# Kernel tuning notes

Measured on AMD Instinct MI355X. Metric: run time of the kernel, lower is better.

The kernel has to match this reference:

```python
import jax, jax.numpy as jnp
import numpy as np
from jax import lax

B, H, L, N, COUT = 16, 128, 8192, 16, 128
NEG_SLOPE = 0.3
BN_EPS = 1e-5


def setup_inputs() -> dict:
    key = jax.random.key(0)
    ks = jax.random.split(key, 20)
    x = jax.random.normal(ks[0], (B, H, L), dtype=jnp.float32)
    # --- S4D parameters ---
    log_dt = jnp.log(0.001) + jax.random.uniform(ks[1], (H,), dtype=jnp.float32) * (jnp.log(0.1) - jnp.log(0.001))
    A_log = jnp.log(0.5 * jnp.ones((H, N), dtype=jnp.float32))  # real part magnitude
    A_imag = jnp.broadcast_to(np.pi * jnp.arange(N, dtype=jnp.float32), (H, N)).copy()
    B_re = jnp.ones((H, N), dtype=jnp.float32)
    B_im = jnp.zeros((H, N), dtype=jnp.float32)
    C_re = jax.random.normal(ks[2], (H, N), dtype=jnp.float32) * (0.5 ** 0.5)
    C_im = jax.random.normal(ks[3], (H, N), dtype=jnp.float32) * (0.5 ** 0.5)
    D = jax.random.normal(ks[4], (H,), dtype=jnp.float32)
    # --- dilated conv branches (kernel_size=3, stride=4) ---
    wscale = 1.0 / np.sqrt(H * 3)
    w1 = jax.random.normal(ks[5], (COUT, H, 3), dtype=jnp.float32) * wscale
    b1 = jnp.zeros((COUT,), dtype=jnp.float32)
    w2 = jax.random.normal(ks[6], (COUT, H, 3), dtype=jnp.float32) * wscale
    b2 = jnp.zeros((COUT,), dtype=jnp.float32)
    w3 = jax.random.normal(ks[7], (COUT, H, 3), dtype=jnp.float32) * wscale
    b3 = jnp.zeros((COUT,), dtype=jnp.float32)
    w4 = jax.random.normal(ks[8], (COUT, H, 3), dtype=jnp.float32) * wscale
    b4 = jnp.zeros((COUT,), dtype=jnp.float32)
    gamma = jnp.ones((COUT,), dtype=jnp.float32)
    beta = jnp.zeros((COUT,), dtype=jnp.float32)
    return dict(x=x, log_dt=log_dt, A_log=A_log, A_imag=A_imag, B_re=B_re, B_im=B_im,
                C_re=C_re, C_im=C_im, D=D, w1=w1, b1=b1, w2=w2, b2=b2, w3=w3, b3=b3,
                w4=w4, b4=b4, gamma=gamma, beta=beta)


def _s4d(x, log_dt, A_log, A_imag, B_re, B_im, C_re, C_im, D):
    # x: (B,H,L). S4D with ZOH discretization, FFT long convolution.
    Lx = x.shape[-1]
    dt = jnp.exp(log_dt)[:, None]                    # (H,1)
    A = -jnp.exp(A_log) + 1j * A_imag                # (H,N)
    dtA = dt * A                                     # (H,N)
    dB = (jnp.exp(dtA) - 1.0) / A * (B_re + 1j * B_im)
    CB = (C_re + 1j * C_im) * dB                     # (H,N)
    l = jnp.arange(Lx, dtype=jnp.float32)
    vand = jnp.exp(dtA[:, :, None] * l)              # (H,N,L) Vandermonde
    K = 2.0 * jnp.real(jnp.einsum('hn,hnl->hl', CB, vand))  # (H,L)
    n = 2 * Lx
    Uf = jnp.fft.rfft(x, n=n)                        # (B,H,L+1)
    Kf = jnp.fft.rfft(K, n=n)                        # (H,L+1)
    y = jnp.fft.irfft(Uf * Kf, n=n)[..., :Lx]
    return y + D[:, None] * x


def _dconv(x, w, b, dil, pad):
    y = lax.conv_general_dilated(x, w, window_strides=(4,), padding=[(pad, pad)],
                                 rhs_dilation=(dil,), dimension_numbers=('NCH', 'OIH', 'NCH'))
    return y + b[:, None]


def _bn(z, gamma, beta):
    # training-mode BatchNorm1d: batch stats over (B, L_out) per channel
    m = jnp.mean(z, axis=(0, 2), keepdims=True)
    v = jnp.var(z, axis=(0, 2), keepdims=True)
    return gamma[:, None] * (z - m) * lax.rsqrt(v + BN_EPS) + beta[:, None]


def _lrelu(z):
    return jnp.where(z >= 0, z, NEG_SLOPE * z)


def reference(x, log_dt, A_log, A_imag, B_re, B_im, C_re, C_im, D,
              w1, b1, w2, b2, w3, b3, w4, b4, gamma, beta):
    y = _s4d(x, log_dt, A_log, A_imag, B_re, B_im, C_re, C_im, D)
    d1 = _bn(_dconv(y, w1, b1, 1, 1), gamma, beta)                 # no activation on branch 1
    d2 = _bn(_lrelu(_dconv(y, w2, b2, 2, 2)), gamma, beta)
    d3 = _bn(_lrelu(_dconv(y, w3, b3, 4, 4)), gamma, beta)
    d4 = _bn(_lrelu(_dconv(y, w4, b4, 8, 8)), gamma, beta)
    return jnp.concatenate([d1, d2, d3, d4], axis=1)               # (B, 4*COUT, L//4)
```

## Files before the change

### kernel.cpp

```cpp
#include <hip/hip_runtime.h>
#include <math.h>

typedef unsigned short u16x8 __attribute__((ext_vector_type(8)));
typedef unsigned short u16x2 __attribute__((ext_vector_type(2)));
typedef short s16x8 __attribute__((ext_vector_type(8)));
typedef float f32x4 __attribute__((ext_vector_type(4)));

__device__ __forceinline__ float bf2f(unsigned short u) {
    union { unsigned int i; float f; } v; v.i = ((unsigned int)u) << 16; return v.f;
}
__device__ __forceinline__ unsigned short f2bf(float f) {
    union { unsigned int i; float f; } v; v.f = f;
    unsigned int r = v.i + 0x7FFFu + ((v.i >> 16) & 1u);
    return (unsigned short)(r >> 16);
}

#define MATS_OFF 16384
#define WB_OFF   548864
#define STAT_OFF 942080
#define Y_OFF    1048576
#define YT_OFF   34603008
#define Z_OFF    Y_OFF

__global__ void precompute_s4d(const float* __restrict__ log_dt,
                               const float* __restrict__ A_log,
                               const float* __restrict__ A_imag,
                               const float* __restrict__ B_re,
                               const float* __restrict__ B_im,
                               const float* __restrict__ C_re,
                               const float* __restrict__ C_im,
                               float* __restrict__ w32,
                               unsigned short* __restrict__ MATS)
{
    const int h = blockIdx.x;
    const int tid = threadIdx.x;
    const double dt = exp((double)log_dt[h]);

    #pragma unroll 1
    for (int it = 0; it < 4; it++) {
        int idx = tid + (it << 8);
        int s = idx >> 5, i = idx & 31;
        int n = s >> 1;
        double Ar = -exp((double)A_log[h * 16 + n]);
        double Ai = (double)A_imag[h * 16 + n];
        double dr = dt * Ar, di = dt * Ai;
        double l = (double)(31 - i);
        double e = exp(l * dr);
        double val = (s & 1) ? e * sin(l * di) : e * cos(l * di);
        MATS[(size_t)h * 2080 + s * 32 + i] = f2bf((float)val);
    }
    #pragma unroll 1
    for (int it = 0; it < 4; it++) {
        int idx = tid + (it << 8);
        int j = idx >> 5, s = idx & 31;
        int n = s >> 1;
        double Ar = -exp((double)A_log[h * 16 + n]);
        double Ai = (double)A_imag[h * 16 + n];
        double dr = dt * Ar, di = dt * Ai;
        double ew = exp(dr);
        double wr = ew * cos(di), wi = ew * sin(di);
        double nr = wr - 1.0, ni = wi;
        double inv = 1.0 / (Ar * Ar + Ai * Ai);
        double tr = (nr * Ar + ni * Ai) * inv;
        double ti = (ni * Ar - nr * Ai) * inv;
        double Br = (double)B_re[h * 16 + n], Bi = (double)B_im[h * 16 + n];
        double dbr = tr * Br - ti * Bi, dbi = tr * Bi + ti * Br;
        double Cr = (double)C_re[h * 16 + n], Ci = (double)C_im[h * 16 + n];
        double cbr = Cr * dbr - Ci * dbi, cbi = Cr * dbi + Ci * dbr;
        double m = (double)(j + 1);
        double e = exp(m * dr);
        double pr = e * cos(m * di), pi = e * sin(m * di);
        double gr = cbr * pr - cbi * pi, gi = cbr * pi + cbi * pr;
        double val = (s & 1) ? -2.0 * gi : 2.0 * gr;
        MATS[(size_t)h * 2080 + 1024 + j * 32 + s] = f2bf((float)val);
    }
    if (tid < 32) {
        double l = (double)tid;
        double acc = 0.0;
        for (int n = 0; n < 16; n++) {
            double Ar = -exp((double)A_log[h * 16 + n]);
            double Ai = (double)A_imag[h * 16 + n];
            double dr = dt * Ar, di = dt * Ai;
            double ew = exp(dr);
            double wr = ew * cos(di), wi = ew * sin(di);
            double nr = wr - 1.0, ni = wi;
            double inv = 1.0 / (Ar * Ar + Ai * Ai);
            double tr = (nr * Ar + ni * Ai) * inv;
            double ti = (ni * Ar - nr * Ai) * inv;
            double Br = (double)B_re[h * 16 + n], Bi = (double)B_im[h * 16 + n];
            double dbr = tr * Br - ti * Bi, dbi = tr * Bi + ti * Br;
            double Cr = (double)C_re[h * 16 + n], Ci = (double)C_im[h * 16 + n];
            double cbr = Cr * dbr - Ci * dbi, cbi = Cr * dbi + Ci * dbr;
            double e = exp(l * dr);
            double wlr = e * cos(l * di), wli = e * sin(l * di);
            acc += cbr * wlr - cbi * wli;
        }
        MATS[(size_t)h * 2080 + 2048 + tid] = f2bf((float)(2.0 * acc));
    }
    if (tid < 16) {
        int n = tid;
        double Ar = -exp((double)A_log[h * 16 + n]);
        double Ai = (double)A_imag[h * 16 + n];
        double dr = dt * Ar, di = dt * Ai;
        double e = exp(32.0 * dr);
        w32[h * 32 + 2 * n]     = (float)(e * cos(32.0 * di));
        w32[h * 32 + 2 * n + 1] = (float)(e * sin(32.0 * di));
    }
}

__global__ void wpack(const float* __restrict__ w1, const float* __restrict__ w2,
                      const float* __restrict__ w3, const float* __restrict__ w4,
                      unsigned short* __restrict__ WB)
{
    int idx = blockIdx.x * 256 + threadIdx.x;
    int br = idx / 49152;
    int r  = idx - br * 49152;
    int co = r / 384;
    int k  = r - co * 384;
    int tap = k >> 7, h = k & 127;
    const float* wp = (br == 0) ? w1 : (br == 1) ? w2 : (br == 2) ? w3 : w4;
    WB[idx] = f2bf(wp[co * 384 + h * 3 + tap]);
}

__global__ __launch_bounds__(256, 2) void s4d_mfma(const float* __restrict__ x,
                                                   const float* __restrict__ w32,
                                                   const unsigned short* __restrict__ MATS,
                                                   const float* __restrict__ Dp,
                                                   unsigned short* __restrict__ yout)
{
    __shared__ unsigned short sXc[256 * 40];
    __shared__ unsigned short sM[3840];
    __shared__ float spow2[256];
    __shared__ unsigned short skr[32];
    __shared__ float scratch[8448];
    const int tid = threadIdx.x;
    const int bh = blockIdx.x;
    const int h = bh & 127;
    const int lane = tid & 63, w = tid >> 6;
    const int ml = lane & 15, kg = lane >> 4;

    float xr[32];
    const float4* xp4 = (const float4*)(x + ((size_t)bh << 13) + (tid << 5));
    #pragma unroll
    for (int i = 0; i < 8; i++) {
        float4 v = xp4[i];
        xr[4 * i] = v.x; xr[4 * i + 1] = v.y; xr[4 * i + 2] = v.z; xr[4 * i + 3] = v.w;
    }
    #pragma unroll
    for (int g = 0; g < 4; g++) {
        u16x8 pk;
        #pragma unroll
        for (int e = 0; e < 8; e++) pk[e] = f2bf(xr[g * 8 + e]);
        *(u16x8*)&sXc[tid * 40 + g * 8] = pk;
    }
    {
        int matv = tid >> 7, r = (tid >> 2) & 31, sg = tid & 3;
        u16x8 v = *(const u16x8*)(MATS + (size_t)h * 2080 + matv * 1024 + r * 32 + sg * 8);
        *(u16x8*)&sM[matv * 2560 + r * 40 + sg * 8] = v;
    }
    if (tid < 4) {
        u16x8 v = *(const u16x8*)(MATS + (size_t)h * 2080 + 2048 + tid * 8);
        *(u16x8*)&skr[tid * 8] = v;
    }
    if (tid < 16) {
        float rr = w32[h * 32 + 2 * tid], ii = w32[h * 32 + 2 * tid + 1];
        #pragma unroll
        for (int k = 0; k < 8; k++) {
            spow2[k * 32 + 2 * tid] = rr; spow2[k * 32 + 2 * tid + 1] = ii;
            float n2r = rr * rr - ii * ii, n2i = 2.f * rr * ii;
            rr = n2r; ii = n2i;
        }
    }
    __syncthreads();
    #pragma unroll
    for (int it = 0; it < 4; it++) {
        int idx = tid + (it << 8);
        int j = idx >> 5, i = idx & 31;
        sM[1280 + j * 40 + i] = (i <= j) ? skr[j - i] : (unsigned short)0;
    }
    __syncthreads();

    f32x4 acc[2][4];
    #pragma unroll
    for (int mt = 0; mt < 2; mt++)
        #pragma unroll
        for (int nt = 0; nt < 4; nt++) acc[mt][nt] = (f32x4)(0.f);
    {
        s16x8 af[2], bfr[4];
        #pragma unroll
        for (int mt = 0; mt < 2; mt++)
            af[mt] = *(const s16x8*)&sM[(mt * 16 + ml) * 40 + kg * 8];
        #pragma unroll
        for (int nt = 0; nt < 4; nt++)
            bfr[nt] = *(const s16x8*)&sXc[(w * 64 + nt * 16 + ml) * 40 + kg * 8];
        #pragma unroll
        for (int mt = 0; mt < 2; mt++)
            #pragma unroll
            for (int nt = 0; nt < 4; nt++)
                acc[mt][nt] = __builtin_amdgcn_mfma_f32_16x16x32_bf16(af[mt], bfr[nt], acc[mt][nt], 0, 0, 0);
    }
    #pragma unroll
    for (int mt = 0; mt < 2; mt++)
        #pragma unroll
        for (int nt = 0; nt < 4; nt++)
            #pragma unroll
            for (int r = 0; r < 4; r++)
                scratch[(mt * 16 + kg * 4 + r) * 264 + (w * 64 + nt * 16 + ml)] = acc[mt][nt][r];
    __syncthreads();
    float zr[16], zi[16];
    #pragma unroll
    for (int n = 0; n < 16; n++) {
        zr[n] = scratch[(2 * n) * 264 + tid];
        zi[n] = scratch[(2 * n + 1) * 264 + tid];
    }
    __syncthreads();

    #pragma unroll 1
    for (int k = 0; k < 8; k++) {
        const int o = 1 << k;
        #pragma unroll
        for (int n = 0; n < 16; n++) {
            scratch[tid * 33 + 2 * n]     = zr[n];
            scratch[tid * 33 + 2 * n + 1] = zi[n];
        }
        __syncthreads();
        if (tid >= o) {
            const float* lp = &scratch[(tid - o) * 33];
            #pragma unroll
            for (int n = 0; n < 16; n++) {
                float lr = lp[2 * n], li = lp[2 * n + 1];
                float mr = spow2[(k << 5) + 2 * n], mi = spow2[(k << 5) + 2 * n + 1];
                zr[n] = fmaf(mr, lr, fmaf(-mi, li, zr[n]));
                zi[n] = fmaf(mr, li, fmaf(mi, lr, zi[n]));
            }
        }
        __syncthreads();
    }
    #pragma unroll
    for (int n = 0; n < 16; n++) {
        scratch[tid * 33 + 2 * n]     = zr[n];
        scratch[tid * 33 + 2 * n + 1] = zi[n];
    }
    __syncthreads();
    if (tid == 0) {
        #pragma unroll
        for (int n = 0; n < 16; n++) { zr[n] = 0.f; zi[n] = 0.f; }
    } else {
        const float* lp = &scratch[(tid - 1) * 33];
        #pragma unroll
        for (int n = 0; n < 16; n++) { zr[n] = lp[2 * n]; zi[n] = lp[2 * n + 1]; }
    }
    __syncthreads();
    {
        unsigned short* sCc = (unsigned short*)scratch;
        #pragma unroll
        for (int g = 0; g < 4; g++) {
            u16x8 pk;
            #pragma unroll
            for (int q = 0; q < 4; q++) {
                pk[2 * q]     = f2bf(zr[g * 4 + q]);
                pk[2 * q + 1] = f2bf(zi[g * 4 + q]);
            }
            *(u16x8*)&sCc[tid * 40 + g * 8] = pk;
        }
    }
    __syncthreads();

    #pragma unroll
    for (int mt = 0; mt < 2; mt++)
        #pragma unroll
        for (int nt = 0; nt < 4; nt++) acc[mt][nt] = (f32x4)(0.f);
    {
        const unsigned short* sCc = (const unsigned short*)scratch;
        s16x8 a1[2], a2[2], bfx[4], bfc[4];
        #pragma unroll
        for (int mt = 0; mt < 2; mt++) {
            a1[mt] = *(const s16x8*)&sM[1280 + (mt * 16 + ml) * 40 + kg * 8];
            a2[mt] = *(const s16x8*)&sM[2560 + (mt * 16 + ml) * 40 + kg * 8];
        }
        #pragma unroll
        for (int nt = 0; nt < 4; nt++) {
            bfx[nt] = *(const s16x8*)&sXc[(w * 64 + nt * 16 + ml) * 40 + kg * 8];
            bfc[nt] = *(const s16x8*)&sCc[(w * 64 + nt * 16 + ml) * 40 + kg * 8];
        }
        #pragma unroll
        for (int mt = 0; mt < 2; mt++)
            #pragma unroll
            for (int nt = 0; nt < 4; nt++) {
                acc[mt][nt] = __builtin_amdgcn_mfma_f32_16x16x32_bf16(a1[mt], bfx[nt], acc[mt][nt], 0, 0, 0);
                acc[mt][nt] = __builtin_amdgcn_mfma_f32_16x16x32_bf16(a2[mt], bfc[nt], acc[mt][nt], 0, 0, 0);
            }
    }
    __syncthreads();
    #pragma unroll
    for (int mt = 0; mt < 2; mt++)
        #pragma unroll
        for (int nt = 0; nt < 4; nt++)
            #pragma unroll
            for (int r = 0; r < 4; r++)
                scratch[(mt * 16 + kg * 4 + r) * 264 + (w * 64 + nt * 16 + ml)] = acc[mt][nt][r];
    __syncthreads();
    const float Dh = Dp[h];
    u16x8* yp = (u16x8*)(yout + ((size_t)bh << 13) + (tid << 5));
    #pragma unroll
    for (int g = 0; g < 4; g++) {
        u16x8 pk;
        #pragma unroll
        for (int e = 0; e < 8; e++) {
            int i = g * 8 + e;
            pk[e] = f2bf(fmaf(Dh, xr[i], scratch[i * 264 + tid]));
        }
        yp[g] = pk;
    }
}

__global__ __launch_bounds__(256) void ytrans(const unsigned short* __restrict__ y,
                                              unsigned short* __restrict__ yT)
{
    __shared__ unsigned short sT[128 * 72];
    const int b = blockIdx.y, g0 = blockIdx.x << 6;
    const int tid = threadIdx.x;
    #pragma unroll
    for (int j = 0; j < 4; j++) {
        int li = tid + (j << 8);
        int h = li >> 3, g8 = (li & 7) << 3;
        u16x8 v = *(const u16x8*)(y + (((size_t)(b * 128 + h)) << 13) + g0 + g8);
        int gp = (g8 + (((h >> 3) & 7) << 3)) & 63;
        *(u16x8*)&sT[h * 72 + gp] = v;
    }
    __syncthreads();
    #pragma unroll
    for (int j = 0; j < 4; j++) {
        int li = tid + (j << 8);
        int g = li >> 4, h8 = (li & 15) << 3;
        u16x8 o;
        #pragma unroll
        for (int e = 0; e < 8; e++) {
            int h = h8 + e;
            int gp = (g + (((h >> 3) & 7) << 3)) & 63;
            o[e] = sT[h * 72 + gp];
        }
        *(u16x8*)(yT + (((size_t)(b * 8192 + g0 + g)) << 7) + h8) = o;
    }
}

__global__ __launch_bounds__(256) void conv_mfma(
    const unsigned short* __restrict__ yT,
    const unsigned short* __restrict__ WB,
    const float* __restrict__ b1, const float* __restrict__ b2,
    const float* __restrict__ b3, const float* __restrict__ b4,
    unsigned short* __restrict__ z)
{
    __shared__ unsigned short sW[128 * 40];
    __shared__ unsigned short sY[128 * 40];
    const int tid = threadIdx.x;
    const int lane = tid & 63, w = tid >> 6;
    const int branch = blockIdx.z, b = blockIdx.y;
    const int t0 = blockIdx.x << 7;
    const int d = 1 << branch;
    const int coH = (w & 1) << 6, tH = (w >> 1) << 6;
    const int ml = lane & 15, kg = lane >> 4;

    f32x4 acc[4][4];
    #pragma unroll
    for (int mt = 0; mt < 4; mt++)
        #pragma unroll
        for (int nt = 0; nt < 4; nt++) acc[mt][nt] = (f32x4)(0.f);

    const unsigned short* WBb = WB + (size_t)branch * 49152;

    for (int kc = 0; kc < 12; kc++) {
        const int tap = kc >> 2, hc = (kc & 3) << 5;
        const int goff = d * (tap - 1);
        __syncthreads();
        #pragma unroll
        for (int j = 0; j < 2; j++) {
            int li = tid + (j << 8);
            int co = li >> 2, kq = (li & 3) << 3;
            u16x8 v = *(const u16x8*)(WBb + (size_t)co * 384 + (kc << 5) + kq);
            *(u16x8*)&sW[co * 40 + kq] = v;
        }
        #pragma unroll
        for (int j = 0; j < 2; j++) {
            int li = tid + (j << 8);
            int n = li >> 2, kq = (li & 3) << 3;
            int g = ((t0 + n) << 2) + goff;
            u16x8 v;
            if ((unsigned)g < 8192u) {
                v = *(const u16x8*)(yT + (((size_t)(b * 8192 + g)) << 7) + hc + kq);
            } else {
                #pragma unroll
                for (int e = 0; e < 8; e++) v[e] = 0;
            }
            *(u16x8*)&sY[n * 40 + kq] = v;
        }
        __syncthreads();
        s16x8 af[4], bfr[4];
        #pragma unroll
        for (int mt = 0; mt < 4; mt++)
            af[mt] = *(const s16x8*)&sW[(coH + mt * 16 + ml) * 40 + (kg << 3)];
        #pragma unroll
        for (int nt = 0; nt < 4; nt++)
            bfr[nt] = *(const s16x8*)&sY[(tH + nt * 16 + ml) * 40 + (kg << 3)];
        #pragma unroll
        for (int mt = 0; mt < 4; mt++)
            #pragma unroll
            for (int nt = 0; nt < 4; nt++)
                acc[mt][nt] = __builtin_amdgcn_mfma_f32_16x16x32_bf16(af[mt], bfr[nt], acc[mt][nt], 0, 0, 0);
    }

    const float* bp = (branch == 0) ? b1 : (branch == 1) ? b2 : (branch == 2) ? b3 : b4;
    #pragma unroll
    for (int mt = 0; mt < 4; mt++) {
        #pragma unroll
        for (int r = 0; r < 4; r++) {
            const int co = coH + mt * 16 + (kg << 2) + r;
            const float bb = bp[co];
            #pragma unroll
            for (int nt = 0; nt < 4; nt++) {
                const int t = t0 + tH + nt * 16 + ml;
                float v = acc[mt][nt][r] + bb;
                if (branch != 0) v = (v >= 0.f) ? v : 0.3f * v;
                z[(((size_t)((branch * 16 + b) * 128 + co)) << 11) + t] = f2bf(v);
            }
        }
    }
}

__global__ __launch_bounds__(256) void bn_stats(const unsigned short* __restrict__ z,
                                                float* __restrict__ stats)
{
    const int bc = blockIdx.x;
    const int branch = bc >> 7, co = bc & 127;
    const int tid = threadIdx.x;
    float s1 = 0.f, s2 = 0.f;
    for (int i = tid; i < 16384; i += 256) {
        int b = i >> 10, tp = (i & 1023) << 1;
        const unsigned short* p = z + (((size_t)((branch * 16 + b) * 128 + co)) << 11) + tp;
        u16x2 v2 = *(const u16x2*)p;
        float a = bf2f(v2[0]), c = bf2f(v2[1]);
        s1 += a + c;
        s2 = fmaf(a, a, fmaf(c, c, s2));
    }
    #pragma unroll
    for (int o = 32; o > 0; o >>= 1) { s1 += __shfl_down(s1, o); s2 += __shfl_down(s2, o); }
    __shared__ float r1[4], r2[4];
    const int lane = tid & 63, wid = tid >> 6;
    if (lane == 0) { r1[wid] = s1; r2[wid] = s2; }
    __syncthreads();
    if (tid == 0) {
        float t1 = r1[0] + r1[1] + r1[2] + r1[3];
        float t2 = r2[0] + r2[1] + r2[2] + r2[3];
        float m = t1 * (1.0f / 32768.0f);
        float var = t2 * (1.0f / 32768.0f) - m * m;
        stats[bc * 2]     = m;
        stats[bc * 2 + 1] = 1.0f / sqrtf(var + 1e-5f);
    }
}

__global__ __launch_bounds__(256) void bn_apply(const unsigned short* __restrict__ z,
                                                const float* __restrict__ stats,
                                                const float* __restrict__ gam,
                                                const float* __restrict__ bet,
                                                float* __restrict__ out)
{
    const size_t idx = (((size_t)blockIdx.x << 8) + threadIdx.x) << 3;
    const int t = (int)(idx & 2047);
    const size_t bc = idx >> 11;
    const int ch = (int)(bc & 511);
    const int b = (int)(bc >> 9);
    const int branch = ch >> 7, co = ch & 127;
    const float m = stats[ch * 2], inv = stats[ch * 2 + 1];
    const float ga = gam[co], be = bet[co];
    const float sc = ga * inv, sh = fmaf(-m, sc, be);
    const unsigned short* zp = z + (((size_t)((branch * 16 + b) * 128 + co)) << 11) + t;
    u16x8 v = *(const u16x8*)zp;
    float4 o0, o1;
    o0.x = fmaf(bf2f(v[0]), sc, sh); o0.y = fmaf(bf2f(v[1]), sc, sh);
    o0.z = fmaf(bf2f(v[2]), sc, sh); o0.w = fmaf(bf2f(v[3]), sc, sh);
    o1.x = fmaf(bf2f(v[4]), sc, sh); o1.y = fmaf(bf2f(v[5]), sc, sh);
    o1.z = fmaf(bf2f(v[6]), sc, sh); o1.w = fmaf(bf2f(v[7]), sc, sh);
    *(float4*)(out + idx)     = o0;
    *(float4*)(out + idx + 4) = o1;
}

extern "C" void kernel_launch(void* const* d_in, const int* in_sizes, int n_in,
                              void* d_out, int out_size, void* d_ws, size_t ws_size,
                              hipStream_t stream) {
    const float* x      = (const float*)d_in[0];
    const float* log_dt = (const float*)d_in[1];
    const float* A_log  = (const float*)d_in[2];
    const float* A_imag = (const float*)d_in[3];
    const float* B_re   = (const float*)d_in[4];
    const float* B_im   = (const float*)d_in[5];
    const float* C_re   = (const float*)d_in[6];
    const float* C_im   = (const float*)d_in[7];
    const float* Dp     = (const float*)d_in[8];
    const float* w1 = (const float*)d_in[9];
    const float* b1 = (const float*)d_in[10];
    const float* w2 = (const float*)d_in[11];
    const float* b2 = (const float*)d_in[12];
    const float* w3 = (const float*)d_in[13];
    const float* b3 = (const float*)d_in[14];
    const float* w4 = (const float*)d_in[15];
    const float* b4 = (const float*)d_in[16];
    const float* gam = (const float*)d_in[17];
    const float* bet = (const float*)d_in[18];

    float* w32p = (float*)d_ws;
    unsigned short* MATSp = (unsigned short*)((char*)d_ws + MATS_OFF);
    unsigned short* WBp = (unsigned short*)((char*)d_ws + WB_OFF);
    float* stats = (float*)((char*)d_ws + STAT_OFF);
    unsigned short* yws = (unsigned short*)((char*)d_ws + Y_OFF);
    unsigned short* yT  = (unsigned short*)((char*)d_ws + YT_OFF);
    unsigned short* zws = (unsigned short*)((char*)d_ws + Z_OFF);
    float* out = (float*)d_out;

    precompute_s4d<<<dim3(128), dim3(256), 0, stream>>>(log_dt, A_log, A_imag,
                                                        B_re, B_im, C_re, C_im, w32p, MATSp);
    wpack<<<dim3(768), dim3(256), 0, stream>>>(w1, w2, w3, w4, WBp);
    s4d_mfma<<<dim3(2048), dim3(256), 0, stream>>>(x, w32p, MATSp, Dp, yws);
    ytrans<<<dim3(128, 16), dim3(256), 0, stream>>>(yws, yT);
    conv_mfma<<<dim3(16, 16, 4), dim3(256), 0, stream>>>(yT, WBp, b1, b2, b3, b4, zws);
    bn_stats<<<dim3(512), dim3(256), 0, stream>>>(zws, stats);
    bn_apply<<<dim3(8192), dim3(256), 0, stream>>>(zws, stats, gam, bet, out);
}
```

Baseline: 284.1 us.

## Fuse BN stats into conv, warp-shuffle scan in S4D, parallelize kernel precompute

Several independent changes. The batch-norm statistics pass is removed: conv_mfma now reduces per-channel sums and sums of squares with shuffles and atomics into a buffer that a new kernel zeroes first, and bn_apply derives mean and variance from it. The S4D block scan now uses wave-level shuffles plus a cross-wave carry combine instead of eight shared-memory rounds with barriers. Other changes: conv weights load straight from global memory into registers instead of through LDS, the precompute kernel spreads its direct-term sum across all threads, and the scratch stride changes. The atomics reorder float accumulation, and computing variance as E[x^2]-m^2 in fp32 may cost some accuracy.

```diff
diff --git a/kernel.cpp b/kernel.cpp
--- a/kernel.cpp
+++ b/kernel.cpp
@@ -2,7 +2,6 @@
 #include <math.h>
 
 typedef unsigned short u16x8 __attribute__((ext_vector_type(8)));
-typedef unsigned short u16x2 __attribute__((ext_vector_type(2)));
 typedef short s16x8 __attribute__((ext_vector_type(8)));
 typedef float f32x4 __attribute__((ext_vector_type(4)));
 
@@ -74,10 +73,12 @@
         double val = (s & 1) ? -2.0 * gi : 2.0 * gr;
         MATS[(size_t)h * 2080 + 1024 + j * 32 + s] = f2bf((float)val);
     }
-    if (tid < 32) {
-        double l = (double)tid;
-        double acc = 0.0;
-        for (int n = 0; n < 16; n++) {
+    {
+        int l = tid >> 3, sub = tid & 7;
+        double accd = 0.0;
+        #pragma unroll 1
+        for (int q = 0; q < 2; q++) {
+            int n = sub * 2 + q;
             double Ar = -exp((double)A_log[h * 16 + n]);
             double Ai = (double)A_imag[h * 16 + n];
             double dr = dt * Ar, di = dt * Ai;
@@ -91,11 +92,15 @@
             double dbr = tr * Br - ti * Bi, dbi = tr * Bi + ti * Br;
             double Cr = (double)C_re[h * 16 + n], Ci = (double)C_im[h * 16 + n];
             double cbr = Cr * dbr - Ci * dbi, cbi = Cr * dbi + Ci * dbr;
-            double e = exp(l * dr);
-            double wlr = e * cos(l * di), wli = e * sin(l * di);
-            acc += cbr * wlr - cbi * wli;
-        }
-        MATS[(size_t)h * 2080 + 2048 + tid] = f2bf((float)(2.0 * acc));
+            double l2 = (double)l;
+            double e = exp(l2 * dr);
+            double wlr = e * cos(l2 * di), wli = e * sin(l2 * di);
+            accd += cbr * wlr - cbi * wli;
+        }
+        float accf = (float)(2.0 * accd);
+        #pragma unroll
+        for (int o = 4; o > 0; o >>= 1) accf += __shfl_down(accf, o, 8);
+        if (sub == 0) MATS[(size_t)h * 2080 + 2048 + l] = f2bf(accf);
     }
     if (tid < 16) {
         int n = tid;
@@ -122,6 +127,13 @@
     WB[idx] = f2bf(wp[co * 384 + h * 3 + tap]);
 }
 
+__global__ void stats_zero(float* __restrict__ stats)
+{
+    int i = threadIdx.x;
+    #pragma unroll
+    for (int k = 0; k < 4; k++) stats[i + k * 256] = 0.f;
+}
+
 __global__ __launch_bounds__(256, 2) void s4d_mfma(const float* __restrict__ x,
                                                    const float* __restrict__ w32,
                                                    const unsigned short* __restrict__ MATS,
@@ -132,7 +144,8 @@
     __shared__ unsigned short sM[3840];
     __shared__ float spow2[256];
     __shared__ unsigned short skr[32];
-    __shared__ float scratch[8448];
+    __shared__ float swc[128];
+    __shared__ float scratch[8320];
     const int tid = threadIdx.x;
     const int bh = blockIdx.x;
     const int h = bh & 127;
@@ -205,52 +218,79 @@
         for (int nt = 0; nt < 4; nt++)
             #pragma unroll
             for (int r = 0; r < 4; r++)
-                scratch[(mt * 16 + kg * 4 + r) * 264 + (w * 64 + nt * 16 + ml)] = acc[mt][nt][r];
+                scratch[(mt * 16 + kg * 4 + r) * 260 + (w * 64 + nt * 16 + ml)] = acc[mt][nt][r];
     __syncthreads();
     float zr[16], zi[16];
     #pragma unroll
     for (int n = 0; n < 16; n++) {
-        zr[n] = scratch[(2 * n) * 264 + tid];
-        zi[n] = scratch[(2 * n + 1) * 264 + tid];
-    }
-    __syncthreads();
+        zr[n] = scratch[(2 * n) * 260 + tid];
+        zi[n] = scratch[(2 * n + 1) * 260 + tid];
+    }
 
     #pragma unroll 1
-    for (int k = 0; k < 8; k++) {
+    for (int k = 0; k < 6; k++) {
         const int o = 1 << k;
+        const bool act = lane >= o;
         #pragma unroll
         for (int n = 0; n < 16; n++) {
-            scratch[tid * 33 + 2 * n]     = zr[n];
-            scratch[tid * 33 + 2 * n + 1] = zi[n];
-        }
-        __syncthreads();
-        if (tid >= o) {
-            const float* lp = &scratch[(tid - o) * 33];
+            float lr = __shfl(zr[n], lane - o);
+            float li = __shfl(zi[n], lane - o);
+            float mr = spow2[(k << 5) + 2 * n], mi = spow2[(k << 5) + 2 * n + 1];
+            float nzr = fmaf(mr, lr, fmaf(-mi, li, zr[n]));
+            float nzi = fmaf(mr, li, fmaf(mi, lr, zi[n]));
+            zr[n] = act ? nzr : zr[n];
+            zi[n] = act ? nzi : zi[n];
+        }
+    }
+    if (lane == 63) {
+        #pragma unroll
+        for (int n = 0; n < 16; n++) {
+            swc[w * 32 + 2 * n]     = zr[n];
+            swc[w * 32 + 2 * n + 1] = zi[n];
+        }
+    }
+    __syncthreads();
+    float qr[16], qi[16];
+    #pragma unroll
+    for (int n = 0; n < 16; n++) { qr[n] = 0.f; qi[n] = 0.f; }
+    #pragma unroll 1
+    for (int a = 0; a < 3; a++) {
+        if (a < w) {
+            int p = w - 1 - a;
             #pragma unroll
             for (int n = 0; n < 16; n++) {
-                float lr = lp[2 * n], li = lp[2 * n + 1];
-                float mr = spow2[(k << 5) + 2 * n], mi = spow2[(k << 5) + 2 * n + 1];
-                zr[n] = fmaf(mr, lr, fmaf(-mi, li, zr[n]));
-                zi[n] = fmaf(mr, li, fmaf(mi, lr, zi[n]));
-            }
-        }
-        __syncthreads();
+                float ar = swc[a * 32 + 2 * n], ai = swc[a * 32 + 2 * n + 1];
+                float mr = 1.f, mi = 0.f;
+                if (p > 0) { mr = spow2[((5 + p) << 5) + 2 * n]; mi = spow2[((5 + p) << 5) + 2 * n + 1]; }
+                qr[n] = fmaf(mr, ar, fmaf(-mi, ai, qr[n]));
+                qi[n] = fmaf(mr, ai, fmaf(mi, ar, qi[n]));
+            }
+        }
+    }
+    float pjr[16], pji[16];
+    #pragma unroll
+    for (int n = 0; n < 16; n++) { pjr[n] = 1.f; pji[n] = 0.f; }
+    #pragma unroll 1
+    for (int k = 0; k < 6; k++) {
+        const bool bit = (lane >> k) & 1;
+        #pragma unroll
+        for (int n = 0; n < 16; n++) {
+            float mr = spow2[(k << 5) + 2 * n], mi = spow2[(k << 5) + 2 * n + 1];
+            float nr2 = pjr[n] * mr - pji[n] * mi;
+            float ni2 = fmaf(pjr[n], mi, pji[n] * mr);
+            pjr[n] = bit ? nr2 : pjr[n];
+            pji[n] = bit ? ni2 : pji[n];
+        }
     }
     #pragma unroll
     for (int n = 0; n < 16; n++) {
-        scratch[tid * 33 + 2 * n]     = zr[n];
-        scratch[tid * 33 + 2 * n + 1] = zi[n];
-    }
-    __syncthreads();
-    if (tid == 0) {
-        #pragma unroll
-        for (int n = 0; n < 16; n++) { zr[n] = 0.f; zi[n] = 0.f; }
-    } else {
-        const float* lp = &scratch[(tid - 1) * 33];
-        #pragma unroll
-        for (int n = 0; n < 16; n++) { zr[n] = lp[2 * n]; zi[n] = lp[2 * n + 1]; }
-    }
-    __syncthreads();
+        float pr = __shfl(zr[n], lane - 1);
+        float pi = __shfl(zi[n], lane - 1);
+        pr = (lane == 0) ? 0.f : pr;
+        pi = (lane == 0) ? 0.f : pi;
+        zr[n] = fmaf(pjr[n], qr[n], fmaf(-pji[n], qi[n], pr));
+        zi[n] = fmaf(pjr[n], qi[n], fmaf(pji[n], qr[n], pi));
+    }
     {
         unsigned short* sCc = (unsigned short*)scratch;
         #pragma unroll
@@ -298,7 +338,7 @@
         for (int nt = 0; nt < 4; nt++)
             #pragma unroll
             for (int r = 0; r < 4; r++)
-                scratch[(mt * 16 + kg * 4 + r) * 264 + (w * 64 + nt * 16 + ml)] = acc[mt][nt][r];
+                scratch[(mt * 16 + kg * 4 + r) * 260 + (w * 64 + nt * 16 + ml)] = acc[mt][nt][r];
     __syncthreads();
     const float Dh = Dp[h];
     u16x8* yp = (u16x8*)(yout + ((size_t)bh << 13) + (tid << 5));
@@ -308,7 +348,7 @@
         #pragma unroll
         for (int e = 0; e < 8; e++) {
             int i = g * 8 + e;
-            pk[e] = f2bf(fmaf(Dh, xr[i], scratch[i * 264 + tid]));
+            pk[e] = f2bf(fmaf(Dh, xr[i], scratch[i * 260 + tid]));
         }
         yp[g] = pk;
     }
@@ -349,9 +389,8 @@
     const unsigned short* __restrict__ WB,
     const float* __restrict__ b1, const float* __restrict__ b2,
     const float* __restrict__ b3, const float* __restrict__ b4,
-    unsigned short* __restrict__ z)
-{
-    __shared__ unsigned short sW[128 * 40];
+    unsigned short* __restrict__ z, float* __restrict__ stats)
+{
     __shared__ unsigned short sY[128 * 40];
     const int tid = threadIdx.x;
     const int lane = tid & 63, w = tid >> 6;
@@ -370,16 +409,14 @@
     const unsigned short* WBb = WB + (size_t)branch * 49152;
 
     for (int kc = 0; kc < 12; kc++) {
-        const int tap = kc >> 2, hc = (kc & 3) << 5;
+        const int tap = kc >> 2;
+        const int hc = (kc & 3) << 5;
         const int goff = d * (tap - 1);
+        s16x8 af[4];
+        #pragma unroll
+        for (int mt = 0; mt < 4; mt++)
+            af[mt] = *(const s16x8*)(WBb + (size_t)(coH + mt * 16 + ml) * 384 + (kc << 5) + (kg << 3));
         __syncthreads();
-        #pragma unroll
-        for (int j = 0; j < 2; j++) {
-            int li = tid + (j << 8);
-            int co = li >> 2, kq = (li & 3) << 3;
-            u16x8 v = *(const u16x8*)(WBb + (size_t)co * 384 + (kc << 5) + kq);
-            *(u16x8*)&sW[co * 40 + kq] = v;
-        }
         #pragma unroll
         for (int j = 0; j < 2; j++) {
             int li = tid + (j << 8);
@@ -395,10 +432,7 @@
             *(u16x8*)&sY[n * 40 + kq] = v;
         }
         __syncthreads();
-        s16x8 af[4], bfr[4];
-        #pragma unroll
-        for (int mt = 0; mt < 4; mt++)
-            af[mt] = *(const s16x8*)&sW[(coH + mt * 16 + ml) * 40 + (kg << 3)];
+        s16x8 bfr[4];
         #pragma unroll
         for (int nt = 0; nt < 4; nt++)
             bfr[nt] = *(const s16x8*)&sY[(tH + nt * 16 + ml) * 40 + (kg << 3)];
@@ -416,45 +450,27 @@
         for (int r = 0; r < 4; r++) {
             const int co = coH + mt * 16 + (kg << 2) + r;
             const float bb = bp[co];
+            float s1 = 0.f, s2 = 0.f;
             #pragma unroll
             for (int nt = 0; nt < 4; nt++) {
                 const int t = t0 + tH + nt * 16 + ml;
                 float v = acc[mt][nt][r] + bb;
                 if (branch != 0) v = (v >= 0.f) ? v : 0.3f * v;
+                s1 += v;
+                s2 = fmaf(v, v, s2);
                 z[(((size_t)((branch * 16 + b) * 128 + co)) << 11) + t] = f2bf(v);
             }
-        }
-    }
-}
-
-__global__ __launch_bounds__(256) void bn_stats(const unsigned short* __restrict__ z,
-                                                float* __restrict__ stats)
-{
-    const int bc = blockIdx.x;
-    const int branch = bc >> 7, co = bc & 127;
-    const int tid = threadIdx.x;
-    float s1 = 0.f, s2 = 0.f;
-    for (int i = tid; i < 16384; i += 256) {
-        int b = i >> 10, tp = (i & 1023) << 1;
-        const unsigned short* p = z + (((size_t)((branch * 16 + b) * 128 + co)) << 11) + tp;
-        u16x2 v2 = *(const u16x2*)p;
-        float a = bf2f(v2[0]), c = bf2f(v2[1]);
-        s1 += a + c;
-        s2 = fmaf(a, a, fmaf(c, c, s2));
-    }
-    #pragma unroll
-    for (int o = 32; o > 0; o >>= 1) { s1 += __shfl_down(s1, o); s2 += __shfl_down(s2, o); }
-    __shared__ float r1[4], r2[4];
-    const int lane = tid & 63, wid = tid >> 6;
-    if (lane == 0) { r1[wid] = s1; r2[wid] = s2; }
-    __syncthreads();
-    if (tid == 0) {
-        float t1 = r1[0] + r1[1] + r1[2] + r1[3];
-        float t2 = r2[0] + r2[1] + r2[2] + r2[3];
-        float m = t1 * (1.0f / 32768.0f);
-        float var = t2 * (1.0f / 32768.0f) - m * m;
-        stats[bc * 2]     = m;
-        stats[bc * 2 + 1] = 1.0f / sqrtf(var + 1e-5f);
+            #pragma unroll
+            for (int o = 8; o > 0; o >>= 1) {
+                s1 += __shfl_down(s1, o, 16);
+                s2 += __shfl_down(s2, o, 16);
+            }
+            if (ml == 0) {
+                const int bc = branch * 128 + co;
+                atomicAdd(&stats[bc * 2], s1);
+                atomicAdd(&stats[bc * 2 + 1], s2);
+            }
+        }
     }
 }
 
@@ -470,7 +486,10 @@
     const int ch = (int)(bc & 511);
     const int b = (int)(bc >> 9);
     const int branch = ch >> 7, co = ch & 127;
-    const float m = stats[ch * 2], inv = stats[ch * 2 + 1];
+    const float s1 = stats[ch * 2], s2 = stats[ch * 2 + 1];
+    const float m = s1 * (1.0f / 32768.0f);
+    const float var = fmaf(-m, m, s2 * (1.0f / 32768.0f));
+    const float inv = rsqrtf(var + 1e-5f);
     const float ga = gam[co], be = bet[co];
     const float sc = ga * inv, sh = fmaf(-m, sc, be);
     const unsigned short* zp = z + (((size_t)((branch * 16 + b) * 128 + co)) << 11) + t;
@@ -519,9 +538,9 @@
     precompute_s4d<<<dim3(128), dim3(256), 0, stream>>>(log_dt, A_log, A_imag,
                                                         B_re, B_im, C_re, C_im, w32p, MATSp);
     wpack<<<dim3(768), dim3(256), 0, stream>>>(w1, w2, w3, w4, WBp);
+    stats_zero<<<dim3(1), dim3(256), 0, stream>>>(stats);
     s4d_mfma<<<dim3(2048), dim3(256), 0, stream>>>(x, w32p, MATSp, Dp, yws);
     ytrans<<<dim3(128, 16), dim3(256), 0, stream>>>(yws, yT);
-    conv_mfma<<<dim3(16, 16, 4), dim3(256), 0, stream>>>(yT, WBp, b1, b2, b3, b4, zws);
-    bn_stats<<<dim3(512), dim3(256), 0, stream>>>(zws, stats);
+    conv_mfma<<<dim3(16, 16, 4), dim3(256), 0, stream>>>(yT, WBp, b1, b2, b3, b4, zws, stats);
     bn_apply<<<dim3(8192), dim3(256), 0, stream>>>(zws, stats, gam, bet, out);
 }
```

Result: slower. 484.6 us (+70.5%).
